# Optimization experiments

Hardware: AMD Instinct MI355X
Metric: run time of the kernel (lower is better)

The kernel has to match this reference:

```python
import jax, jax.numpy as jnp
import numpy as np

B, L, D, H, DEPTH, K = 16, 2048, 256, 8, 2, 7
HD = D // H
SCALE = HD ** -0.5


def _ln(x, g, b, eps=1e-5):
    m = x.mean(-1, keepdims=True)
    v = ((x - m) ** 2).mean(-1, keepdims=True)
    return (x - m) * jax.lax.rsqrt(v + eps) * g + b


def _nat_attn(x, qkv_w, qkv_b, proj_w, proj_b):
    # Neighborhood attention 1D: window of K tokens centered on each token,
    # clamped at sequence edges (NATTEN semantics, dilation=1).
    b, l, d = x.shape
    qkv = (x @ qkv_w + qkv_b).reshape(b, l, 3, H, HD).transpose(2, 0, 3, 1, 4)  # [3,B,H,L,hd]
    q, k, v = qkv[0] * SCALE, qkv[1], qkv[2]
    starts = jnp.clip(jnp.arange(l) - K // 2, 0, l - K)          # [L]
    idx = starts[:, None] + jnp.arange(K)                        # [L,K]
    kn = k[:, :, idx]                                            # [B,H,L,K,hd]
    vn = v[:, :, idx]
    attn = jax.nn.softmax(jnp.einsum('bhld,bhlkd->bhlk', q, kn), axis=-1)
    out = jnp.einsum('bhlk,bhlkd->bhld', attn, vn)               # [B,H,L,hd]
    out = out.transpose(0, 2, 1, 3).reshape(b, l, d)
    return out @ proj_w + proj_b


def _mlp(x, w1, b1, w2, b2):
    return jax.nn.gelu(x @ w1 + b1, approximate=False) @ w2 + b2


def setup_inputs() -> dict:
    key = jax.random.key(0)
    ks = jax.random.split(key, 8)
    s = 0.02
    return {
        'x': jax.random.normal(ks[0], (B, L, D), jnp.float32),
        'ln1_g': jnp.ones((DEPTH, D), jnp.float32),
        'ln1_b': jnp.zeros((DEPTH, D), jnp.float32),
        'qkv_w': jax.random.normal(ks[1], (DEPTH, D, 3 * D), jnp.float32) * s,
        'qkv_b': jnp.zeros((DEPTH, 3 * D), jnp.float32),
        'proj_w': jax.random.normal(ks[2], (DEPTH, D, D), jnp.float32) * s,
        'proj_b': jnp.zeros((DEPTH, D), jnp.float32),
        'ln2_g': jnp.ones((DEPTH, D), jnp.float32),
        'ln2_b': jnp.zeros((DEPTH, D), jnp.float32),
        'fc1_w': jax.random.normal(ks[3], (DEPTH, D, 4 * D), jnp.float32) * s,
        'fc1_b': jnp.zeros((DEPTH, 4 * D), jnp.float32),
        'fc2_w': jax.random.normal(ks[4], (DEPTH, 4 * D, D), jnp.float32) * s,
        'fc2_b': jnp.zeros((DEPTH, D), jnp.float32),
        'conv_w': jax.random.normal(ks[5], (2 * D, D, 3), jnp.float32) * s,  # OIH
        'dn_g': jnp.ones((2 * D,), jnp.float32),
        'dn_b': jnp.zeros((2 * D,), jnp.float32),
    }


def reference(x, ln1_g, ln1_b, qkv_w, qkv_b, proj_w, proj_b,
              ln2_g, ln2_b, fc1_w, fc1_b, fc2_w, fc2_b,
              conv_w, dn_g, dn_b):
    for i in range(DEPTH):
        h = _nat_attn(_ln(x, ln1_g[i], ln1_b[i]), qkv_w[i], qkv_b[i], proj_w[i], proj_b[i])
        x = x + h
        x = x + _mlp(_ln(x, ln2_g[i], ln2_b[i]), fc1_w[i], fc1_b[i], fc2_w[i], fc2_b[i])
    # ConvDownsampler: Conv1d(D, 2D, k=3, s=2, p=1, bias=False) + LayerNorm
    xc = x.transpose(0, 2, 1)  # [B,C,L]
    y = jax.lax.conv_general_dilated(xc, conv_w, window_strides=(2,),
                                     padding=[(1, 1)],
                                     dimension_numbers=('NCH', 'OIH', 'NCH'))
    y = y.transpose(0, 2, 1)   # [B, L//2, 2D]
    y = _ln(y, dn_g, dn_b)
    return (y, x)
```

## Files before the change

### kernel.cpp

```cpp
#include <hip/hip_runtime.h>

typedef unsigned short u16;
typedef __attribute__((ext_vector_type(8))) short bf16x8;
typedef __attribute__((ext_vector_type(4))) float f32x4;

__device__ __forceinline__ float bf2f(u16 u) { return __uint_as_float(((unsigned)u) << 16); }
__device__ __forceinline__ u16 f2bf(float f) {
    unsigned u = __float_as_uint(f);
    return (u16)((u + 0x7FFFu + ((u >> 16) & 1u)) >> 16);
}

__device__ __forceinline__ float gelu_fast(float v) {
    float u = v * (1.5957691216057308f + 0.07135481282700722f * v * v);
    return v * (1.f / (1.f + __expf(-u)));
}

__device__ __forceinline__ void load_lds16(const u16* g, u16* l) {
    __builtin_amdgcn_global_load_lds(
        (const __attribute__((address_space(1))) unsigned int*)g,
        (__attribute__((address_space(3))) unsigned int*)l,
        16, 0, 0);
}

template<int EPI>
__global__ __launch_bounds__(256) void gemm_kernel(
    const u16* __restrict__ A, const u16* __restrict__ Wt,
    const float* __restrict__ bias, const float* __restrict__ res,
    void* __restrict__ outp, int M, int N, int K)
{
    __shared__ __align__(16) u16 As[128 * 64];
    __shared__ __align__(16) u16 Bs[128 * 64];
    const int tid  = threadIdx.x;
    const int lane = tid & 63;
    const int wave = tid >> 6;
    const int row0 = blockIdx.x * 128;
    const int col0 = blockIdx.y * 128;
    const int wr = (wave >> 1) * 64;
    const int wc = (wave & 1) * 64;
    const int lr = lane & 15;
    const int q  = lane >> 4;

    f32x4 acc[4][4];
#pragma unroll
    for (int i = 0; i < 4; ++i)
#pragma unroll
        for (int j = 0; j < 4; ++j) acc[i][j] = (f32x4){0.f, 0.f, 0.f, 0.f};

    const int strow  = tid >> 3;
    const int schunk = (tid & 7) ^ (strow & 7);
    const u16* ag = A  + (size_t)(row0 + strow) * K + schunk * 8;
    const u16* bg = Wt + (size_t)(col0 + strow) * K + schunk * 8;
    const size_t rstep32 = (size_t)32 * K;
    u16* alp = As + tid * 8;
    u16* blp = Bs + tid * 8;

    for (int k0 = 0; k0 < K; k0 += 64) {
        __syncthreads();
#pragma unroll
        for (int s = 0; s < 4; ++s) {
            load_lds16(ag + s * rstep32 + k0, alp + s * 2048);
            load_lds16(bg + s * rstep32 + k0, blp + s * 2048);
        }
        __syncthreads();
#pragma unroll
        for (int kk = 0; kk < 2; ++kk) {
            bf16x8 af[4], bfv[4];
#pragma unroll
            for (int i = 0; i < 4; ++i) {
                const int r = wr + i * 16 + lr;
                af[i] = *(const bf16x8*)(As + r * 64 + (((kk * 4 + q) ^ (r & 7)) * 8));
            }
#pragma unroll
            for (int j = 0; j < 4; ++j) {
                const int r = wc + j * 16 + lr;
                bfv[j] = *(const bf16x8*)(Bs + r * 64 + (((kk * 4 + q) ^ (r & 7)) * 8));
            }
#pragma unroll
            for (int i = 0; i < 4; ++i)
#pragma unroll
                for (int j = 0; j < 4; ++j)
                    acc[i][j] = __builtin_amdgcn_mfma_f32_16x16x32_bf16(af[i], bfv[j], acc[i][j], 0, 0, 0);
        }
    }

#pragma unroll
    for (int i = 0; i < 4; ++i) {
        const int rbase = row0 + wr + i * 16 + (lane >> 4) * 4;
#pragma unroll
        for (int j = 0; j < 4; ++j) {
            const int col = col0 + wc + j * 16 + lr;
            const float bv = (EPI == 3) ? 0.f : bias[col];
#pragma unroll
            for (int r = 0; r < 4; ++r) {
                const int row = rbase + r;
                float v = acc[i][j][r] + bv;
                if (EPI == 1) {
                    v += res[(size_t)row * N + col];
                    ((float*)outp)[(size_t)row * N + col] = v;
                } else {
                    if (EPI == 2) v = gelu_fast(v);
                    ((u16*)outp)[(size_t)row * N + col] = f2bf(v);
                }
            }
        }
    }
}

__global__ __launch_bounds__(256) void ln_f2b_kernel(
    const float* __restrict__ x, const float* __restrict__ g,
    const float* __restrict__ be, u16* __restrict__ out)
{
    const int lane = threadIdx.x & 63;
    const int row  = blockIdx.x * 4 + (threadIdx.x >> 6);
    const float4 a = *(const float4*)(x + (size_t)row * 256 + lane * 4);
    float v[4] = {a.x, a.y, a.z, a.w};
    float s = v[0] + v[1] + v[2] + v[3];
#pragma unroll
    for (int m = 1; m < 64; m <<= 1) s += __shfl_xor(s, m);
    const float mean = s * (1.f / 256.f);
    float s2 = 0.f;
#pragma unroll
    for (int e = 0; e < 4; ++e) { float d = v[e] - mean; s2 += d * d; }
#pragma unroll
    for (int m = 1; m < 64; m <<= 1) s2 += __shfl_xor(s2, m);
    const float rstd = rsqrtf(s2 * (1.f / 256.f) + 1e-5f);
    const float4 gg = *(const float4*)(g + lane * 4);
    const float4 bb = *(const float4*)(be + lane * 4);
    ushort4 o;
    o.x = f2bf((v[0] - mean) * rstd * gg.x + bb.x);
    o.y = f2bf((v[1] - mean) * rstd * gg.y + bb.y);
    o.z = f2bf((v[2] - mean) * rstd * gg.z + bb.z);
    o.w = f2bf((v[3] - mean) * rstd * gg.w + bb.w);
    *(ushort4*)(out + (size_t)row * 256 + lane * 4) = o;
}

__global__ __launch_bounds__(256) void ln_b2f_kernel(
    const u16* __restrict__ x, const float* __restrict__ g,
    const float* __restrict__ be, float* __restrict__ out)
{
    const int lane = threadIdx.x & 63;
    const int row  = blockIdx.x * 4 + (threadIdx.x >> 6);
    const u16* xr = x + (size_t)row * 512 + lane * 8;
    float v[8];
#pragma unroll
    for (int e = 0; e < 8; e += 4) {
        ushort4 a = *(const ushort4*)(xr + e);
        v[e] = bf2f(a.x); v[e+1] = bf2f(a.y); v[e+2] = bf2f(a.z); v[e+3] = bf2f(a.w);
    }
    float s = 0.f;
#pragma unroll
    for (int e = 0; e < 8; ++e) s += v[e];
#pragma unroll
    for (int m = 1; m < 64; m <<= 1) s += __shfl_xor(s, m);
    const float mean = s * (1.f / 512.f);
    float s2 = 0.f;
#pragma unroll
    for (int e = 0; e < 8; ++e) { float d = v[e] - mean; s2 += d * d; }
#pragma unroll
    for (int m = 1; m < 64; m <<= 1) s2 += __shfl_xor(s2, m);
    const float rstd = rsqrtf(s2 * (1.f / 512.f) + 1e-5f);
    float* orow = out + (size_t)row * 512 + lane * 8;
#pragma unroll
    for (int e = 0; e < 8; e += 4) {
        float4 o;
        o.x = (v[e]   - mean) * rstd * g[lane*8+e]   + be[lane*8+e];
        o.y = (v[e+1] - mean) * rstd * g[lane*8+e+1] + be[lane*8+e+1];
        o.z = (v[e+2] - mean) * rstd * g[lane*8+e+2] + be[lane*8+e+2];
        o.w = (v[e+3] - mean) * rstd * g[lane*8+e+3] + be[lane*8+e+3];
        *(float4*)(orow + e) = o;
    }
}

__global__ __launch_bounds__(256) void attn_kernel(
    const u16* __restrict__ qkv, u16* __restrict__ out)
{
    const int lane  = threadIdx.x & 63;
    const int token = blockIdx.x * 4 + (threadIdx.x >> 6);
    const int b = token >> 11;
    const int l = token & 2047;
    const int h = lane >> 3;
    const int s = lane & 7;
    const int off = h * 32 + s * 4;

    ushort4 q4 = *(const ushort4*)(qkv + (size_t)token * 768 + off);
    const float scale = 0.17677669529663687f;
    float q0 = bf2f(q4.x), q1 = bf2f(q4.y), q2 = bf2f(q4.z), q3 = bf2f(q4.w);

    int start = l - 3;
    start = start < 0 ? 0 : (start > 2041 ? 2041 : start);
    const u16* kbase = qkv + ((size_t)(b << 11) + start) * 768 + 256 + off;

    float sc[7], vv[7][4];
#pragma unroll
    for (int j = 0; j < 7; ++j) {
        const u16* kp = kbase + (size_t)j * 768;
        ushort4 k4 = *(const ushort4*)kp;
        ushort4 v4 = *(const ushort4*)(kp + 256);
        float d = q0 * bf2f(k4.x) + q1 * bf2f(k4.y) + q2 * bf2f(k4.z) + q3 * bf2f(k4.w);
        d += __shfl_xor(d, 1); d += __shfl_xor(d, 2); d += __shfl_xor(d, 4);
        sc[j] = d * scale;
        vv[j][0] = bf2f(v4.x); vv[j][1] = bf2f(v4.y); vv[j][2] = bf2f(v4.z); vv[j][3] = bf2f(v4.w);
    }
    float mx = sc[0];
#pragma unroll
    for (int j = 1; j < 7; ++j) mx = fmaxf(mx, sc[j]);
    float p[7], sum = 0.f;
#pragma unroll
    for (int j = 0; j < 7; ++j) { p[j] = expf(sc[j] - mx); sum += p[j]; }
    const float inv = 1.f / sum;
    float o0 = 0, o1 = 0, o2 = 0, o3 = 0;
#pragma unroll
    for (int j = 0; j < 7; ++j) {
        o0 += p[j] * vv[j][0]; o1 += p[j] * vv[j][1];
        o2 += p[j] * vv[j][2]; o3 += p[j] * vv[j][3];
    }
    ushort4 o;
    o.x = f2bf(o0 * inv); o.y = f2bf(o1 * inv); o.z = f2bf(o2 * inv); o.w = f2bf(o3 * inv);
    *(ushort4*)(out + (size_t)token * 256 + off) = o;
}

__global__ void transpose_kernel(const float* __restrict__ in, u16* __restrict__ out,
                                 int K, int N, int total)
{
    int idx = blockIdx.x * 256 + threadIdx.x;
    if (idx >= total) return;
    int k = idx % K;
    int n = (idx / K) % N;
    int d = idx / (K * N);
    out[idx] = f2bf(in[(size_t)d * K * N + (size_t)k * N + n]);
}

__global__ void convw_kernel(const float* __restrict__ in, u16* __restrict__ out)
{
    int idx = blockIdx.x * 256 + threadIdx.x;
    int r  = idx % 768;
    int co = idx / 768;
    int t  = r / 256;
    int ci = r % 256;
    out[idx] = f2bf(in[(size_t)co * 768 + (size_t)ci * 3 + t]);
}

__global__ __launch_bounds__(256) void im2col_kernel(
    const float* __restrict__ x, u16* __restrict__ x2, int r0)
{
    int idx = blockIdx.x * 256 + threadIdx.x;
    int c4  = idx & 63;
    int t   = (idx >> 6) % 3;
    int rl  = idx / 192;
    int row = r0 + rl;
    int b   = row >> 10;
    int lo  = row & 1023;
    int l   = 2 * lo + t - 1;
    ushort4 o = {0, 0, 0, 0};
    if (l >= 0 && l < 2048) {
        float4 val = *(const float4*)(x + ((size_t)(b << 11) + l) * 256 + c4 * 4);
        o.x = f2bf(val.x); o.y = f2bf(val.y); o.z = f2bf(val.z); o.w = f2bf(val.w);
    }
    *(ushort4*)(x2 + (size_t)rl * 768 + t * 256 + c4 * 4) = o;
}

extern "C" void kernel_launch(void* const* d_in, const int* in_sizes, int n_in,
                              void* d_out, int out_size, void* d_ws, size_t ws_size,
                              hipStream_t stream)
{
    const float* x_in   = (const float*)d_in[0];
    const float* ln1_g  = (const float*)d_in[1];
    const float* ln1_b  = (const float*)d_in[2];
    const float* qkv_w  = (const float*)d_in[3];
    const float* qkv_b  = (const float*)d_in[4];
    const float* proj_w = (const float*)d_in[5];
    const float* proj_b = (const float*)d_in[6];
    const float* ln2_g  = (const float*)d_in[7];
    const float* ln2_b  = (const float*)d_in[8];
    const float* fc1_w  = (const float*)d_in[9];
    const float* fc1_b  = (const float*)d_in[10];
    const float* fc2_w  = (const float*)d_in[11];
    const float* fc2_b  = (const float*)d_in[12];
    const float* conv_w = (const float*)d_in[13];
    const float* dn_g   = (const float*)d_in[14];
    const float* dn_b   = (const float*)d_in[15];

    float* xbuf = (float*)d_out + 8388608;
    u16*   xn   = (u16*)d_out;

    char* ws = (char*)d_ws;
    const size_t MB = 1024ull * 1024;
    u16* qkv_wt  = (u16*)ws;
    u16* proj_wt = qkv_wt  + 2 * 768 * 256;
    u16* fc1_wt  = proj_wt + 2 * 256 * 256;
    u16* fc2_wt  = fc1_wt  + 2 * 1024 * 256;
    u16* conv_wt = fc2_wt  + 2 * 256 * 1024;
    u16* S       = (u16*)(ws + 4 * MB);

    const size_t R = ws_size > 4 * MB ? ws_size - 4 * MB : 0;
    int nb = 16;    while (nb > 1 && (size_t)nb * 4 * MB > R) nb >>= 1;
    int Mf = 32768; while (Mf > 2048 && (size_t)Mf * 2048 > R) Mf >>= 1;
    int Mc = 16384; while (Mc > 2048 && (size_t)Mc * 2560 > R) Mc >>= 1;

    transpose_kernel<<<(2*256*768 + 255) / 256, 256, 0, stream>>>(qkv_w,  qkv_wt,  256, 768, 2*256*768);
    transpose_kernel<<<(2*256*256 + 255) / 256, 256, 0, stream>>>(proj_w, proj_wt, 256, 256, 2*256*256);
    transpose_kernel<<<(2*256*1024 + 255) / 256, 256, 0, stream>>>(fc1_w, fc1_wt,  256, 1024, 2*256*1024);
    transpose_kernel<<<(2*1024*256 + 255) / 256, 256, 0, stream>>>(fc2_w, fc2_wt,  1024, 256, 2*1024*256);
    convw_kernel<<<(512*768) / 256, 256, 0, stream>>>(conv_w, conv_wt);

    hipMemcpyAsync(xbuf, x_in, 32768ull * 256 * 4, hipMemcpyDeviceToDevice, stream);

    for (int layer = 0; layer < 2; ++layer) {
        const float* l1g = ln1_g + layer * 256;
        const float* l1b = ln1_b + layer * 256;
        const float* l2g = ln2_g + layer * 256;
        const float* l2b = ln2_b + layer * 256;
        const u16*   qwt = qkv_wt  + (size_t)layer * 768 * 256;
        const float* qb  = qkv_b   + layer * 768;
        const u16*   pwt = proj_wt + (size_t)layer * 256 * 256;
        const float* pb  = proj_b  + layer * 256;
        const u16*   f1w = fc1_wt  + (size_t)layer * 1024 * 256;
        const float* f1b = fc1_b   + layer * 1024;
        const u16*   f2w = fc2_wt  + (size_t)layer * 256 * 1024;
        const float* f2b = fc2_b   + layer * 256;

        ln_f2b_kernel<<<8192, 256, 0, stream>>>(xbuf, l1g, l1b, xn);
        {
            const int Mg = nb * 2048;
            u16* qkvc  = S;
            u16* atnoc = S + (size_t)Mg * 768;
            for (int g = 0; g < 16 / nb; ++g) {
                const size_t t0 = (size_t)g * Mg;
                gemm_kernel<0><<<dim3(Mg / 128, 6), 256, 0, stream>>>(
                    xn + t0 * 256, qwt, qb, nullptr, qkvc, Mg, 768, 256);
                attn_kernel<<<Mg / 4, 256, 0, stream>>>(qkvc, atnoc);
                gemm_kernel<1><<<dim3(Mg / 128, 2), 256, 0, stream>>>(
                    atnoc, pwt, pb, xbuf + t0 * 256, xbuf + t0 * 256, Mg, 256, 256);
            }
        }
        ln_f2b_kernel<<<8192, 256, 0, stream>>>(xbuf, l2g, l2b, xn);
        {
            u16* hbuf = S;
            for (int q = 0; q < 32768 / Mf; ++q) {
                const size_t r0 = (size_t)q * Mf;
                gemm_kernel<2><<<dim3(Mf / 128, 8), 256, 0, stream>>>(
                    xn + r0 * 256, f1w, f1b, nullptr, hbuf, Mf, 1024, 256);
                gemm_kernel<1><<<dim3(Mf / 128, 2), 256, 0, stream>>>(
                    hbuf, f2w, f2b, xbuf + r0 * 256, xbuf + r0 * 256, Mf, 256, 1024);
            }
        }
    }

    {
        u16* x2c = S;
        u16* ycc = S + (size_t)Mc * 768;
        for (int c = 0; c < 16384 / Mc; ++c) {
            const int r0 = c * Mc;
            im2col_kernel<<<3 * Mc / 4, 256, 0, stream>>>(xbuf, x2c, r0);
            gemm_kernel<3><<<dim3(Mc / 128, 4), 256, 0, stream>>>(
                x2c, conv_wt, nullptr, nullptr, ycc, Mc, 512, 768);
            ln_b2f_kernel<<<Mc / 4, 256, 0, stream>>>(
                ycc, dn_g, dn_b, (float*)d_out + (size_t)r0 * 512);
        }
    }
}
```

Baseline: 496.8 us.

## Vectorize GEMM epilogue, tile weight transpose, drop input copy, use fast exp

Swaps the MFMA operand order so each lane holds four consecutive output columns, which lets the GEMM epilogue do float4 bias, residual and output accesses instead of scalar strided stores. Replaces the naive weight transpose with an LDS-tiled version that makes coalesced vector reads and writes. Removes the device-to-device copy of the input by having the first layer read x directly and write its residual into xbuf. Switches softmax to __expf. These cut memory traffic and store instruction count, at the cost of slightly lower exp accuracy.

```diff
diff --git a/kernel.cpp b/kernel.cpp
--- a/kernel.cpp
+++ b/kernel.cpp
@@ -79,28 +79,37 @@
             for (int i = 0; i < 4; ++i)
 #pragma unroll
                 for (int j = 0; j < 4; ++j)
-                    acc[i][j] = __builtin_amdgcn_mfma_f32_16x16x32_bf16(af[i], bfv[j], acc[i][j], 0, 0, 0);
-        }
-    }
-
-#pragma unroll
-    for (int i = 0; i < 4; ++i) {
-        const int rbase = row0 + wr + i * 16 + (lane >> 4) * 4;
-#pragma unroll
-        for (int j = 0; j < 4; ++j) {
-            const int col = col0 + wc + j * 16 + lr;
-            const float bv = (EPI == 3) ? 0.f : bias[col];
-#pragma unroll
-            for (int r = 0; r < 4; ++r) {
-                const int row = rbase + r;
-                float v = acc[i][j][r] + bv;
-                if (EPI == 1) {
-                    v += res[(size_t)row * N + col];
-                    ((float*)outp)[(size_t)row * N + col] = v;
-                } else {
-                    if (EPI == 2) v = gelu_fast(v);
-                    ((u16*)outp)[(size_t)row * N + col] = f2bf(v);
+                    acc[i][j] = __builtin_amdgcn_mfma_f32_16x16x32_bf16(bfv[j], af[i], acc[i][j], 0, 0, 0);
+        }
+    }
+
+#pragma unroll
+    for (int j = 0; j < 4; ++j) {
+        const int cb = col0 + wc + j * 16 + q * 4;
+        float4 bv;
+        if (EPI == 3) { bv.x = bv.y = bv.z = bv.w = 0.f; }
+        else          { bv = *(const float4*)(bias + cb); }
+#pragma unroll
+        for (int i = 0; i < 4; ++i) {
+            const int row = row0 + wr + i * 16 + lr;
+            float v0 = acc[i][j][0] + bv.x;
+            float v1 = acc[i][j][1] + bv.y;
+            float v2 = acc[i][j][2] + bv.z;
+            float v3 = acc[i][j][3] + bv.w;
+            if (EPI == 1) {
+                const size_t o = (size_t)row * N + cb;
+                const float4 rr = *(const float4*)(res + o);
+                float4 ov;
+                ov.x = v0 + rr.x; ov.y = v1 + rr.y; ov.z = v2 + rr.z; ov.w = v3 + rr.w;
+                *(float4*)((float*)outp + o) = ov;
+            } else {
+                if (EPI == 2) {
+                    v0 = gelu_fast(v0); v1 = gelu_fast(v1);
+                    v2 = gelu_fast(v2); v3 = gelu_fast(v3);
                 }
+                ushort4 ov;
+                ov.x = f2bf(v0); ov.y = f2bf(v1); ov.z = f2bf(v2); ov.w = f2bf(v3);
+                *(ushort4*)((u16*)outp + (size_t)row * N + cb) = ov;
             }
         }
     }
@@ -206,7 +215,7 @@
     for (int j = 1; j < 7; ++j) mx = fmaxf(mx, sc[j]);
     float p[7], sum = 0.f;
 #pragma unroll
-    for (int j = 0; j < 7; ++j) { p[j] = expf(sc[j] - mx); sum += p[j]; }
+    for (int j = 0; j < 7; ++j) { p[j] = __expf(sc[j] - mx); sum += p[j]; }
     const float inv = 1.f / sum;
     float o0 = 0, o1 = 0, o2 = 0, o3 = 0;
 #pragma unroll
@@ -219,15 +228,22 @@
     *(ushort4*)(out + (size_t)token * 256 + off) = o;
 }
 
-__global__ void transpose_kernel(const float* __restrict__ in, u16* __restrict__ out,
-                                 int K, int N, int total)
-{
-    int idx = blockIdx.x * 256 + threadIdx.x;
-    if (idx >= total) return;
-    int k = idx % K;
-    int n = (idx / K) % N;
-    int d = idx / (K * N);
-    out[idx] = f2bf(in[(size_t)d * K * N + (size_t)k * N + n]);
+__global__ __launch_bounds__(256) void transpose_kernel(
+    const float* __restrict__ in, u16* __restrict__ out, int K, int N)
+{
+    __shared__ float t[32][33];
+    const int n0 = blockIdx.x * 32;
+    const int k0 = blockIdx.y * 32;
+    const int d  = blockIdx.z;
+    const int tr = threadIdx.x >> 3;
+    const int tc = (threadIdx.x & 7) * 4;
+    const float4 a = *(const float4*)(in + ((size_t)d * K + k0 + tr) * N + n0 + tc);
+    t[tc + 0][tr] = a.x; t[tc + 1][tr] = a.y; t[tc + 2][tr] = a.z; t[tc + 3][tr] = a.w;
+    __syncthreads();
+    ushort4 o;
+    o.x = f2bf(t[tr][tc + 0]); o.y = f2bf(t[tr][tc + 1]);
+    o.z = f2bf(t[tr][tc + 2]); o.w = f2bf(t[tr][tc + 3]);
+    *(ushort4*)(out + ((size_t)d * N + n0 + tr) * K + k0 + tc) = o;
 }
 
 __global__ void convw_kernel(const float* __restrict__ in, u16* __restrict__ out)
@@ -297,13 +313,11 @@
     int Mf = 32768; while (Mf > 2048 && (size_t)Mf * 2048 > R) Mf >>= 1;
     int Mc = 16384; while (Mc > 2048 && (size_t)Mc * 2560 > R) Mc >>= 1;
 
-    transpose_kernel<<<(2*256*768 + 255) / 256, 256, 0, stream>>>(qkv_w,  qkv_wt,  256, 768, 2*256*768);
-    transpose_kernel<<<(2*256*256 + 255) / 256, 256, 0, stream>>>(proj_w, proj_wt, 256, 256, 2*256*256);
-    transpose_kernel<<<(2*256*1024 + 255) / 256, 256, 0, stream>>>(fc1_w, fc1_wt,  256, 1024, 2*256*1024);
-    transpose_kernel<<<(2*1024*256 + 255) / 256, 256, 0, stream>>>(fc2_w, fc2_wt,  1024, 256, 2*1024*256);
-    convw_kernel<<<(512*768) / 256, 256, 0, stream>>>(conv_w, conv_wt);
-
-    hipMemcpyAsync(xbuf, x_in, 32768ull * 256 * 4, hipMemcpyDeviceToDevice, stream);
+    transpose_kernel<<<dim3(768 / 32, 256 / 32, 2), 256, 0, stream>>>(qkv_w,  qkv_wt,  256, 768);
+    transpose_kernel<<<dim3(256 / 32, 256 / 32, 2), 256, 0, stream>>>(proj_w, proj_wt, 256, 256);
+    transpose_kernel<<<dim3(1024 / 32, 256 / 32, 2), 256, 0, stream>>>(fc1_w, fc1_wt, 256, 1024);
+    transpose_kernel<<<dim3(256 / 32, 1024 / 32, 2), 256, 0, stream>>>(fc2_w, fc2_wt, 1024, 256);
+    convw_kernel<<<(512 * 768) / 256, 256, 0, stream>>>(conv_w, conv_wt);
 
     for (int layer = 0; layer < 2; ++layer) {
         const float* l1g = ln1_g + layer * 256;
@@ -319,7 +333,9 @@
         const u16*   f2w = fc2_wt  + (size_t)layer * 256 * 1024;
         const float* f2b = fc2_b   + layer * 256;
 
-        ln_f2b_kernel<<<8192, 256, 0, stream>>>(xbuf, l1g, l1b, xn);
+        const float* xsrc = (layer == 0) ? x_in : xbuf;
+
+        ln_f2b_kernel<<<8192, 256, 0, stream>>>(xsrc, l1g, l1b, xn);
         {
             const int Mg = nb * 2048;
             u16* qkvc  = S;
@@ -330,14 +346,14 @@
                     xn + t0 * 256, qwt, qb, nullptr, qkvc, Mg, 768, 256);
                 attn_kernel<<<Mg / 4, 256, 0, stream>>>(qkvc, atnoc);
                 gemm_kernel<1><<<dim3(Mg / 128, 2), 256, 0, stream>>>(
-                    atnoc, pwt, pb, xbuf + t0 * 256, xbuf + t0 * 256, Mg, 256, 256);
+                    atnoc, pwt, pb, xsrc + t0 * 256, xbuf + t0 * 256, Mg, 256, 256);
             }
         }
         ln_f2b_kernel<<<8192, 256, 0, stream>>>(xbuf, l2g, l2b, xn);
         {
             u16* hbuf = S;
-            for (int q = 0; q < 32768 / Mf; ++q) {
-                const size_t r0 = (size_t)q * Mf;
+            for (int qq = 0; qq < 32768 / Mf; ++qq) {
+                const size_t r0 = (size_t)qq * Mf;
                 gemm_kernel<2><<<dim3(Mf / 128, 8), 256, 0, stream>>>(
                     xn + r0 * 256, f1w, f1b, nullptr, hbuf, Mf, 1024, 256);
                 gemm_kernel<1><<<dim3(Mf / 128, 2), 256, 0, stream>>>(
```

Measured after the change: 508.3 us. +2.3%, slower.
